# Kernel optimization log

Hardware: AMD Instinct MI355X
Metric: run time of the kernel (lower is better)

Reference implementation:

```python
import jax, jax.numpy as jnp
import numpy as np

BATCH, D_INNER, DT_RANK, N = 256, 5120, 160, 16

def _softplus_thresh(z, threshold=20.0):
    # softplus(z) with beta=1; linear above threshold (matches ttnn.softplus(parameter1=1, parameter2=20))
    return jnp.where(z > threshold, z, jax.nn.softplus(z))

def setup_inputs() -> dict:
    key = jax.random.key(0)
    ks = jax.random.split(key, 9)
    s = lambda d: 1.0 / np.sqrt(d)
    return {
        "x": jax.random.normal(ks[0], (1, 1, BATCH, D_INNER), jnp.float32),
        "h": jax.random.normal(ks[1], (BATCH, D_INNER, N), jnp.float32) * 0.1,
        "W_delta": jax.random.normal(ks[2], (D_INNER, DT_RANK), jnp.float32) * s(D_INNER),
        "W_dt": jax.random.normal(ks[3], (DT_RANK, D_INNER), jnp.float32) * s(DT_RANK),
        "b_dt": jax.random.normal(ks[4], (D_INNER,), jnp.float32) * 0.1,
        "A_log": jax.random.uniform(ks[5], (D_INNER, N), jnp.float32, 0.0, 1.5),
        "W_B": jax.random.normal(ks[6], (D_INNER, N), jnp.float32) * s(D_INNER),
        "W_C": jax.random.normal(ks[7], (D_INNER, N), jnp.float32) * s(D_INNER),
        "D": jax.random.normal(ks[8], (D_INNER,), jnp.float32),
    }

def reference(x, h, W_delta, W_dt, b_dt, A_log, W_B, W_C, D):
    # x: (1,1,B,d_inner) single decode step; h: (B,d_inner,n) SSM state
    xb = x.reshape(BATCH, D_INNER)                           # (B, d)
    # delta = softplus(x @ W_delta @ W_dt + b_dt)           -> (B, d)
    dt = _softplus_thresh((xb @ W_delta) @ W_dt + b_dt)
    A = -jnp.exp(A_log)                                      # (d, n)
    abar = jnp.exp(dt[:, :, None] * A[None, :, :])           # (B, d, n)
    Bp = xb @ W_B                                            # (B, n)
    # bbar * x: delta * B * x, broadcast over state dim
    bx = (dt * xb)[:, :, None] * Bp[:, None, :]              # (B, d, n)
    h_new = abar * h + bx                                    # (B, d, n) new hidden state
    C = xb @ W_C                                             # (B, n)
    y = jnp.einsum("bdn,bn->bd", h_new, C) + xb * D          # readout + skip (D)
    return y.reshape(1, 1, BATCH, D_INNER)
```

## Files before the change

kernel.cpp:

```cpp
#include <hip/hip_runtime.h>
#include <math.h>

#define BATCH 256
#define DIN   5120
#define RANK  160
#define NS    16
#define NCAT  192
#define NSPLIT 40

__global__ __launch_bounds__(256) void k1a_gemm(
    const float* __restrict__ x, const float* __restrict__ Wd,
    const float* __restrict__ WB, const float* __restrict__ WC,
    float* __restrict__ psum)
{
    __shared__ float xT[32][64];
    __shared__ float Wt[32][64];
    const int t  = threadIdx.x;
    const int m0 = blockIdx.x * 64;
    const int n0 = blockIdx.y * 64;
    const int z  = blockIdx.z;
    const int k0 = z * 128;
    const int tm = (t >> 4) * 4;
    const int tn = (t & 15) * 4;

    const int lm  = t >> 2;
    const int lk  = (t & 3) * 8;
    const int ln  = t & 63;
    const int lkb = (t >> 6) * 8;

    const float* wsrc; int wstr;
    {
        const int c = n0 + ln;
        if (c < RANK)            { wsrc = Wd + c;                wstr = RANK; }
        else if (c < RANK + NS)  { wsrc = WB + (c - RANK);       wstr = NS;   }
        else                     { wsrc = WC + (c - RANK - NS);  wstr = NS;   }
    }

    float acc[4][4] = {{0.f}};

    for (int ks = 0; ks < 4; ++ks) {
        const int kb = k0 + ks * 32;
        {
            const float* src = x + (size_t)(m0 + lm) * DIN + kb + lk;
            const float4 a0 = *(const float4*)src;
            const float4 a1 = *(const float4*)(src + 4);
            xT[lk+0][lm]=a0.x; xT[lk+1][lm]=a0.y; xT[lk+2][lm]=a0.z; xT[lk+3][lm]=a0.w;
            xT[lk+4][lm]=a1.x; xT[lk+5][lm]=a1.y; xT[lk+6][lm]=a1.z; xT[lk+7][lm]=a1.w;
        }
        {
            const float* wp = wsrc + (size_t)(kb + lkb) * wstr;
            #pragma unroll
            for (int i = 0; i < 8; ++i) { Wt[lkb + i][ln] = *wp; wp += wstr; }
        }
        __syncthreads();
        #pragma unroll
        for (int k = 0; k < 32; ++k) {
            const float4 a = *(const float4*)&xT[k][tm];
            const float4 b = *(const float4*)&Wt[k][tn];
            acc[0][0] += a.x*b.x; acc[0][1] += a.x*b.y; acc[0][2] += a.x*b.z; acc[0][3] += a.x*b.w;
            acc[1][0] += a.y*b.x; acc[1][1] += a.y*b.y; acc[1][2] += a.y*b.z; acc[1][3] += a.y*b.w;
            acc[2][0] += a.z*b.x; acc[2][1] += a.z*b.y; acc[2][2] += a.z*b.z; acc[2][3] += a.z*b.w;
            acc[3][0] += a.w*b.x; acc[3][1] += a.w*b.y; acc[3][2] += a.w*b.z; acc[3][3] += a.w*b.w;
        }
        __syncthreads();
    }

    float* dst = psum + (size_t)z * (BATCH * NCAT);
    #pragma unroll
    for (int i = 0; i < 4; ++i) {
        const int gm = m0 + tm + i;
        float4 o; o.x = acc[i][0]; o.y = acc[i][1]; o.z = acc[i][2]; o.w = acc[i][3];
        *(float4*)&dst[(size_t)gm * NCAT + n0 + tn] = o;
    }
}

__global__ __launch_bounds__(256) void k1r_reduce(
    const float* __restrict__ psum,
    float* __restrict__ P, float* __restrict__ Bp, float* __restrict__ Cc)
{
    const int o = blockIdx.x * 256 + threadIdx.x;
    float s = 0.f;
    #pragma unroll 8
    for (int z = 0; z < NSPLIT; ++z) s += psum[(size_t)z * (BATCH * NCAT) + o];
    const int gm = o / NCAT;
    const int gc = o - gm * NCAT;
    if (gc < RANK)           P [gm * RANK + gc]             = s;
    else if (gc < RANK + NS) Bp[gm * NS   + gc - RANK]      = s;
    else                     Cc[gm * NS   + gc - RANK - NS] = s;
}

__device__ __forceinline__ float softplus20(float z)
{
    if (z > 20.f) return z;
    return fmaxf(z, 0.f) + log1pf(__expf(-fabsf(z)));
}

__global__ __launch_bounds__(256) void k3_ssm(
    const float* __restrict__ P, const float* __restrict__ Wdt,
    const float* __restrict__ bdt, const float* __restrict__ x,
    const float* __restrict__ h, const float* __restrict__ A_log,
    const float* __restrict__ Bp, const float* __restrict__ Cc,
    const float* __restrict__ Dv, float* __restrict__ y)
{
    __shared__ float sP[16 * RANK];
    __shared__ float Bt[32][64];
    __shared__ float sdt[16][64];

    const int t    = threadIdx.x;
    const int lane = t & 63;
    const int wv   = t >> 6;
    const int c0   = blockIdx.x * 64;
    const int b0   = blockIdx.y * 16;

    {
        const float* Pb = P + (size_t)b0 * RANK;
        #pragma unroll
        for (int i = 0; i < 10; ++i) sP[i * 256 + t] = Pb[i * 256 + t];

        const int ln  = lane;
        const int lkb = wv * 8;
        float acc[4] = {0.f, 0.f, 0.f, 0.f};

        for (int ks = 0; ks < 5; ++ks) {
            const int kb = ks * 32;
            {
                const float* wp = Wdt + (size_t)(kb + lkb) * DIN + c0 + ln;
                #pragma unroll
                for (int i = 0; i < 8; ++i) Bt[lkb + i][ln] = wp[(size_t)i * DIN];
            }
            __syncthreads();
            #pragma unroll
            for (int k = 0; k < 32; ++k) {
                const float w = Bt[k][lane];
                acc[0] += sP[(wv * 4 + 0) * RANK + kb + k] * w;
                acc[1] += sP[(wv * 4 + 1) * RANK + kb + k] * w;
                acc[2] += sP[(wv * 4 + 2) * RANK + kb + k] * w;
                acc[3] += sP[(wv * 4 + 3) * RANK + kb + k] * w;
            }
            __syncthreads();
        }

        const float bz = bdt[c0 + lane];
        #pragma unroll
        for (int i = 0; i < 4; ++i)
            sdt[wv * 4 + i][lane] = softplus20(acc[i] + bz);
    }
    __syncthreads();

    const int v = lane & 3;
    const int j = lane >> 2;

    float4 A2q[4]; float dvq[4];
    #pragma unroll
    for (int q = 0; q < 4; ++q) {
        const int c = c0 + q * 16 + j;
        const float4 al = *(const float4*)(A_log + (size_t)c * NS + v * 4);
        A2q[q].x = -1.442695041f * __expf(al.x);
        A2q[q].y = -1.442695041f * __expf(al.y);
        A2q[q].z = -1.442695041f * __expf(al.z);
        A2q[q].w = -1.442695041f * __expf(al.w);
        dvq[q] = Dv[c];
    }

    #pragma unroll
    for (int g = 0; g < 2; ++g) {
        const int bl0 = wv * 4 + g * 2;
        const int gb0 = b0 + bl0;
        const int gb1 = gb0 + 1;

        const size_t hb0 = ((size_t)gb0 * DIN + c0) * NS;
        const size_t hb1 = ((size_t)gb1 * DIN + c0) * NS;
        const float4 h00 = *(const float4*)(h + hb0 +   0 + lane * 4);
        const float4 h01 = *(const float4*)(h + hb0 + 256 + lane * 4);
        const float4 h02 = *(const float4*)(h + hb0 + 512 + lane * 4);
        const float4 h03 = *(const float4*)(h + hb0 + 768 + lane * 4);
        const float4 h10 = *(const float4*)(h + hb1 +   0 + lane * 4);
        const float4 h11 = *(const float4*)(h + hb1 + 256 + lane * 4);
        const float4 h12 = *(const float4*)(h + hb1 + 512 + lane * 4);
        const float4 h13 = *(const float4*)(h + hb1 + 768 + lane * 4);
        const float  xr0 = x[(size_t)gb0 * DIN + c0 + lane];
        const float  xr1 = x[(size_t)gb1 * DIN + c0 + lane];
        const float4 B40 = *(const float4*)(Bp + gb0 * NS + v * 4);
        const float4 C40 = *(const float4*)(Cc + gb0 * NS + v * 4);
        const float4 B41 = *(const float4*)(Bp + gb1 * NS + v * 4);
        const float4 C41 = *(const float4*)(Cc + gb1 * NS + v * 4);

        float res0[4];
        #pragma unroll
        for (int q = 0; q < 4; ++q) {
            const float dtv = sdt[bl0][q * 16 + j];
            const float xv  = __shfl(xr0, q * 16 + j, 64);
            const float dtx = dtv * xv;
            const float4 hv = (q == 0) ? h00 : (q == 1) ? h01 : (q == 2) ? h02 : h03;
            float s;
            s  = (exp2f(dtv * A2q[q].x) * hv.x + dtx * B40.x) * C40.x;
            s += (exp2f(dtv * A2q[q].y) * hv.y + dtx * B40.y) * C40.y;
            s += (exp2f(dtv * A2q[q].z) * hv.z + dtx * B40.z) * C40.z;
            s += (exp2f(dtv * A2q[q].w) * hv.w + dtx * B40.w) * C40.w;
            if (v == 0) s += xv * dvq[q];
            res0[q] = s;
        }

        float res1[4];
        #pragma unroll
        for (int q = 0; q < 4; ++q) {
            const float dtv = sdt[bl0 + 1][q * 16 + j];
            const float xv  = __shfl(xr1, q * 16 + j, 64);
            const float dtx = dtv * xv;
            const float4 hv = (q == 0) ? h10 : (q == 1) ? h11 : (q == 2) ? h12 : h13;
            float s;
            s  = (exp2f(dtv * A2q[q].x) * hv.x + dtx * B41.x) * C41.x;
            s += (exp2f(dtv * A2q[q].y) * hv.y + dtx * B41.y) * C41.y;
            s += (exp2f(dtv * A2q[q].z) * hv.z + dtx * B41.z) * C41.z;
            s += (exp2f(dtv * A2q[q].w) * hv.w + dtx * B41.w) * C41.w;
            if (v == 0) s += xv * dvq[q];
            res1[q] = s;
        }

        #pragma unroll
        for (int q = 0; q < 4; ++q) {
            res0[q] += __shfl_xor(res0[q], 1, 64);
            res0[q] += __shfl_xor(res0[q], 2, 64);
            res1[q] += __shfl_xor(res1[q], 1, 64);
            res1[q] += __shfl_xor(res1[q], 2, 64);
        }
        const float out0 = (v == 0) ? res0[0] : (v == 1) ? res0[1]
                         : (v == 2) ? res0[2] : res0[3];
        const float out1 = (v == 0) ? res1[0] : (v == 1) ? res1[1]
                         : (v == 2) ? res1[2] : res1[3];
        y[(size_t)gb0 * DIN + c0 + v * 16 + j] = out0;
        y[(size_t)gb1 * DIN + c0 + v * 16 + j] = out1;
    }
}

extern "C" void kernel_launch(void* const* d_in, const int* in_sizes, int n_in,
                              void* d_out, int out_size, void* d_ws, size_t ws_size,
                              hipStream_t stream)
{
    const float* x     = (const float*)d_in[0];
    const float* h     = (const float*)d_in[1];
    const float* Wd    = (const float*)d_in[2];
    const float* Wdt   = (const float*)d_in[3];
    const float* bdt   = (const float*)d_in[4];
    const float* A_log = (const float*)d_in[5];
    const float* WB    = (const float*)d_in[6];
    const float* WC    = (const float*)d_in[7];
    const float* Dv    = (const float*)d_in[8];
    float* out = (float*)d_out;

    float* psum = (float*)d_ws;
    float* P    = psum + (size_t)NSPLIT * BATCH * NCAT;
    float* Bp   = P  + BATCH * RANK;
    float* Cc   = Bp + BATCH * NS;

    k1a_gemm  <<<dim3(4, 3, NSPLIT), 256, 0, stream>>>(x, Wd, WB, WC, psum);
    k1r_reduce<<<dim3(NCAT),         256, 0, stream>>>(psum, P, Bp, Cc);
    k3_ssm    <<<dim3(80, 16),       256, 0, stream>>>(P, Wdt, bdt, x, h, A_log,
                                                       Bp, Cc, Dv, out);
}
```

Measured before the change: 174.1 us.

## Split dt projection into its own tiled GEMM and slim the SSM kernel

Moves the P @ W_dt projection and softplus out of the SSM kernel into a separate register-tiled 64x64 GEMM that writes dt to workspace, reusing the psum buffer. Before, each of 16 batch blocks re-read W_dt per column tile. The SSM kernel now handles 2 batches per wave with no shared memory, giving a larger grid. The split-K factor of the first GEMM doubles and the reduce kernel uses smaller blocks to add parallelism. The cost is an extra launch and a round trip of dt through global memory.

```diff
diff --git a/kernel.cpp b/kernel.cpp
--- a/kernel.cpp
+++ b/kernel.cpp
@@ -6,7 +6,7 @@
 #define RANK  160
 #define NS    16
 #define NCAT  192
-#define NSPLIT 40
+#define NSPLIT 80
 
 __global__ __launch_bounds__(256) void k1a_gemm(
     const float* __restrict__ x, const float* __restrict__ Wd,
@@ -19,7 +19,7 @@
     const int m0 = blockIdx.x * 64;
     const int n0 = blockIdx.y * 64;
     const int z  = blockIdx.z;
-    const int k0 = z * 128;
+    const int k0 = z * 64;
     const int tm = (t >> 4) * 4;
     const int tn = (t & 15) * 4;
 
@@ -38,7 +38,7 @@
 
     float acc[4][4] = {{0.f}};
 
-    for (int ks = 0; ks < 4; ++ks) {
+    for (int ks = 0; ks < 2; ++ks) {
         const int kb = k0 + ks * 32;
         {
             const float* src = x + (size_t)(m0 + lm) * DIN + kb + lk;
@@ -74,11 +74,11 @@
     }
 }
 
-__global__ __launch_bounds__(256) void k1r_reduce(
+__global__ __launch_bounds__(128) void k1r_reduce(
     const float* __restrict__ psum,
     float* __restrict__ P, float* __restrict__ Bp, float* __restrict__ Cc)
 {
-    const int o = blockIdx.x * 256 + threadIdx.x;
+    const int o = blockIdx.x * 128 + threadIdx.x;
     float s = 0.f;
     #pragma unroll 8
     for (int z = 0; z < NSPLIT; ++z) s += psum[(size_t)z * (BATCH * NCAT) + o];
@@ -95,60 +95,98 @@
     return fmaxf(z, 0.f) + log1pf(__expf(-fabsf(z)));
 }
 
+__global__ __launch_bounds__(256) void k2_dt(
+    const float* __restrict__ P, const float* __restrict__ Wdt,
+    const float* __restrict__ bdt, float* __restrict__ dtw)
+{
+    __shared__ float aT[32][64];
+    __shared__ float Bt[32][64];
+
+    const int t  = threadIdx.x;
+    const int c0 = blockIdx.x * 64;
+    const int b0 = blockIdx.y * 64;
+
+    const int tm = (t >> 4) * 4;
+    const int tn = (t & 15) * 4;
+    const int lm  = t >> 2;
+    const int lk  = (t & 3) * 8;
+    const int ln  = t & 63;
+    const int lkb = (t >> 6) * 8;
+
+    float acc[4][4] = {{0.f}};
+
+    for (int ks = 0; ks < 5; ++ks) {
+        const int kb = ks * 32;
+        {
+            const float* src = P + (size_t)(b0 + lm) * RANK + kb + lk;
+            const float4 a0 = *(const float4*)src;
+            const float4 a1 = *(const float4*)(src + 4);
+            aT[lk+0][lm]=a0.x; aT[lk+1][lm]=a0.y; aT[lk+2][lm]=a0.z; aT[lk+3][lm]=a0.w;
+            aT[lk+4][lm]=a1.x; aT[lk+5][lm]=a1.y; aT[lk+6][lm]=a1.z; aT[lk+7][lm]=a1.w;
+        }
+        {
+            const float* wp = Wdt + (size_t)(kb + lkb) * DIN + c0 + ln;
+            #pragma unroll
+            for (int i = 0; i < 8; ++i) { Bt[lkb + i][ln] = wp[(size_t)i * DIN]; }
+        }
+        __syncthreads();
+        #pragma unroll
+        for (int k = 0; k < 32; ++k) {
+            const float4 a = *(const float4*)&aT[k][tm];
+            const float4 b = *(const float4*)&Bt[k][tn];
+            acc[0][0] += a.x*b.x; acc[0][1] += a.x*b.y; acc[0][2] += a.x*b.z; acc[0][3] += a.x*b.w;
+            acc[1][0] += a.y*b.x; acc[1][1] += a.y*b.y; acc[1][2] += a.y*b.z; acc[1][3] += a.y*b.w;
+            acc[2][0] += a.z*b.x; acc[2][1] += a.z*b.y; acc[2][2] += a.z*b.z; acc[2][3] += a.z*b.w;
+            acc[3][0] += a.w*b.x; acc[3][1] += a.w*b.y; acc[3][2] += a.w*b.z; acc[3][3] += a.w*b.w;
+        }
+        __syncthreads();
+    }
+
+    const float4 bz = *(const float4*)&bdt[c0 + tn];
+    #pragma unroll
+    for (int i = 0; i < 4; ++i) {
+        float4 o;
+        o.x = softplus20(acc[i][0] + bz.x);
+        o.y = softplus20(acc[i][1] + bz.y);
+        o.z = softplus20(acc[i][2] + bz.z);
+        o.w = softplus20(acc[i][3] + bz.w);
+        *(float4*)&dtw[(size_t)(b0 + tm + i) * DIN + c0 + tn] = o;
+    }
+}
+
 __global__ __launch_bounds__(256) void k3_ssm(
-    const float* __restrict__ P, const float* __restrict__ Wdt,
-    const float* __restrict__ bdt, const float* __restrict__ x,
+    const float* __restrict__ dtw, const float* __restrict__ x,
     const float* __restrict__ h, const float* __restrict__ A_log,
     const float* __restrict__ Bp, const float* __restrict__ Cc,
     const float* __restrict__ Dv, float* __restrict__ y)
 {
-    __shared__ float sP[16 * RANK];
-    __shared__ float Bt[32][64];
-    __shared__ float sdt[16][64];
-
     const int t    = threadIdx.x;
     const int lane = t & 63;
     const int wv   = t >> 6;
     const int c0   = blockIdx.x * 64;
-    const int b0   = blockIdx.y * 16;
-
-    {
-        const float* Pb = P + (size_t)b0 * RANK;
-        #pragma unroll
-        for (int i = 0; i < 10; ++i) sP[i * 256 + t] = Pb[i * 256 + t];
-
-        const int ln  = lane;
-        const int lkb = wv * 8;
-        float acc[4] = {0.f, 0.f, 0.f, 0.f};
-
-        for (int ks = 0; ks < 5; ++ks) {
-            const int kb = ks * 32;
-            {
-                const float* wp = Wdt + (size_t)(kb + lkb) * DIN + c0 + ln;
-                #pragma unroll
-                for (int i = 0; i < 8; ++i) Bt[lkb + i][ln] = wp[(size_t)i * DIN];
-            }
-            __syncthreads();
-            #pragma unroll
-            for (int k = 0; k < 32; ++k) {
-                const float w = Bt[k][lane];
-                acc[0] += sP[(wv * 4 + 0) * RANK + kb + k] * w;
-                acc[1] += sP[(wv * 4 + 1) * RANK + kb + k] * w;
-                acc[2] += sP[(wv * 4 + 2) * RANK + kb + k] * w;
-                acc[3] += sP[(wv * 4 + 3) * RANK + kb + k] * w;
-            }
-            __syncthreads();
-        }
-
-        const float bz = bdt[c0 + lane];
-        #pragma unroll
-        for (int i = 0; i < 4; ++i)
-            sdt[wv * 4 + i][lane] = softplus20(acc[i] + bz);
-    }
-    __syncthreads();
-
-    const int v = lane & 3;
-    const int j = lane >> 2;
+    const int gb0  = blockIdx.y * 8 + wv * 2;
+    const int gb1  = gb0 + 1;
+    const int v    = lane & 3;
+    const int j    = lane >> 2;
+
+    const size_t hb0 = ((size_t)gb0 * DIN + c0) * NS;
+    const size_t hb1 = ((size_t)gb1 * DIN + c0) * NS;
+    const float4 h00 = *(const float4*)(h + hb0 +   0 + lane * 4);
+    const float4 h01 = *(const float4*)(h + hb0 + 256 + lane * 4);
+    const float4 h02 = *(const float4*)(h + hb0 + 512 + lane * 4);
+    const float4 h03 = *(const float4*)(h + hb0 + 768 + lane * 4);
+    const float4 h10 = *(const float4*)(h + hb1 +   0 + lane * 4);
+    const float4 h11 = *(const float4*)(h + hb1 + 256 + lane * 4);
+    const float4 h12 = *(const float4*)(h + hb1 + 512 + lane * 4);
+    const float4 h13 = *(const float4*)(h + hb1 + 768 + lane * 4);
+    const float  xr0 = x  [(size_t)gb0 * DIN + c0 + lane];
+    const float  xr1 = x  [(size_t)gb1 * DIN + c0 + lane];
+    const float  dr0 = dtw[(size_t)gb0 * DIN + c0 + lane];
+    const float  dr1 = dtw[(size_t)gb1 * DIN + c0 + lane];
+    const float4 B40 = *(const float4*)(Bp + gb0 * NS + v * 4);
+    const float4 C40 = *(const float4*)(Cc + gb0 * NS + v * 4);
+    const float4 B41 = *(const float4*)(Bp + gb1 * NS + v * 4);
+    const float4 C41 = *(const float4*)(Cc + gb1 * NS + v * 4);
 
     float4 A2q[4]; float dvq[4];
     #pragma unroll
@@ -162,75 +200,51 @@
         dvq[q] = Dv[c];
     }
 
-    #pragma unroll
-    for (int g = 0; g < 2; ++g) {
-        const int bl0 = wv * 4 + g * 2;
-        const int gb0 = b0 + bl0;
-        const int gb1 = gb0 + 1;
-
-        const size_t hb0 = ((size_t)gb0 * DIN + c0) * NS;
-        const size_t hb1 = ((size_t)gb1 * DIN + c0) * NS;
-        const float4 h00 = *(const float4*)(h + hb0 +   0 + lane * 4);
-        const float4 h01 = *(const float4*)(h + hb0 + 256 + lane * 4);
-        const float4 h02 = *(const float4*)(h + hb0 + 512 + lane * 4);
-        const float4 h03 = *(const float4*)(h + hb0 + 768 + lane * 4);
-        const float4 h10 = *(const float4*)(h + hb1 +   0 + lane * 4);
-        const float4 h11 = *(const float4*)(h + hb1 + 256 + lane * 4);
-        const float4 h12 = *(const float4*)(h + hb1 + 512 + lane * 4);
-        const float4 h13 = *(const float4*)(h + hb1 + 768 + lane * 4);
-        const float  xr0 = x[(size_t)gb0 * DIN + c0 + lane];
-        const float  xr1 = x[(size_t)gb1 * DIN + c0 + lane];
-        const float4 B40 = *(const float4*)(Bp + gb0 * NS + v * 4);
-        const float4 C40 = *(const float4*)(Cc + gb0 * NS + v * 4);
-        const float4 B41 = *(const float4*)(Bp + gb1 * NS + v * 4);
-        const float4 C41 = *(const float4*)(Cc + gb1 * NS + v * 4);
-
-        float res0[4];
-        #pragma unroll
-        for (int q = 0; q < 4; ++q) {
-            const float dtv = sdt[bl0][q * 16 + j];
-            const float xv  = __shfl(xr0, q * 16 + j, 64);
-            const float dtx = dtv * xv;
-            const float4 hv = (q == 0) ? h00 : (q == 1) ? h01 : (q == 2) ? h02 : h03;
-            float s;
-            s  = (exp2f(dtv * A2q[q].x) * hv.x + dtx * B40.x) * C40.x;
-            s += (exp2f(dtv * A2q[q].y) * hv.y + dtx * B40.y) * C40.y;
-            s += (exp2f(dtv * A2q[q].z) * hv.z + dtx * B40.z) * C40.z;
-            s += (exp2f(dtv * A2q[q].w) * hv.w + dtx * B40.w) * C40.w;
-            if (v == 0) s += xv * dvq[q];
-            res0[q] = s;
-        }
-
-        float res1[4];
-        #pragma unroll
-        for (int q = 0; q < 4; ++q) {
-            const float dtv = sdt[bl0 + 1][q * 16 + j];
-            const float xv  = __shfl(xr1, q * 16 + j, 64);
-            const float dtx = dtv * xv;
-            const float4 hv = (q == 0) ? h10 : (q == 1) ? h11 : (q == 2) ? h12 : h13;
-            float s;
-            s  = (exp2f(dtv * A2q[q].x) * hv.x + dtx * B41.x) * C41.x;
-            s += (exp2f(dtv * A2q[q].y) * hv.y + dtx * B41.y) * C41.y;
-            s += (exp2f(dtv * A2q[q].z) * hv.z + dtx * B41.z) * C41.z;
-            s += (exp2f(dtv * A2q[q].w) * hv.w + dtx * B41.w) * C41.w;
-            if (v == 0) s += xv * dvq[q];
-            res1[q] = s;
-        }
-
-        #pragma unroll
-        for (int q = 0; q < 4; ++q) {
-            res0[q] += __shfl_xor(res0[q], 1, 64);
-            res0[q] += __shfl_xor(res0[q], 2, 64);
-            res1[q] += __shfl_xor(res1[q], 1, 64);
-            res1[q] += __shfl_xor(res1[q], 2, 64);
-        }
-        const float out0 = (v == 0) ? res0[0] : (v == 1) ? res0[1]
-                         : (v == 2) ? res0[2] : res0[3];
-        const float out1 = (v == 0) ? res1[0] : (v == 1) ? res1[1]
-                         : (v == 2) ? res1[2] : res1[3];
-        y[(size_t)gb0 * DIN + c0 + v * 16 + j] = out0;
-        y[(size_t)gb1 * DIN + c0 + v * 16 + j] = out1;
-    }
+    float res0[4];
+    #pragma unroll
+    for (int q = 0; q < 4; ++q) {
+        const float dtv = __shfl(dr0, q * 16 + j, 64);
+        const float xv  = __shfl(xr0, q * 16 + j, 64);
+        const float dtx = dtv * xv;
+        const float4 hv = (q == 0) ? h00 : (q == 1) ? h01 : (q == 2) ? h02 : h03;
+        float s;
+        s  = (exp2f(dtv * A2q[q].x) * hv.x + dtx * B40.x) * C40.x;
+        s += (exp2f(dtv * A2q[q].y) * hv.y + dtx * B40.y) * C40.y;
+        s += (exp2f(dtv * A2q[q].z) * hv.z + dtx * B40.z) * C40.z;
+        s += (exp2f(dtv * A2q[q].w) * hv.w + dtx * B40.w) * C40.w;
+        if (v == 0) s += xv * dvq[q];
+        res0[q] = s;
+    }
+
+    float res1[4];
+    #pragma unroll
+    for (int q = 0; q < 4; ++q) {
+        const float dtv = __shfl(dr1, q * 16 + j, 64);
+        const float xv  = __shfl(xr1, q * 16 + j, 64);
+        const float dtx = dtv * xv;
+        const float4 hv = (q == 0) ? h10 : (q == 1) ? h11 : (q == 2) ? h12 : h13;
+        float s;
+        s  = (exp2f(dtv * A2q[q].x) * hv.x + dtx * B41.x) * C41.x;
+        s += (exp2f(dtv * A2q[q].y) * hv.y + dtx * B41.y) * C41.y;
+        s += (exp2f(dtv * A2q[q].z) * hv.z + dtx * B41.z) * C41.z;
+        s += (exp2f(dtv * A2q[q].w) * hv.w + dtx * B41.w) * C41.w;
+        if (v == 0) s += xv * dvq[q];
+        res1[q] = s;
+    }
+
+    #pragma unroll
+    for (int q = 0; q < 4; ++q) {
+        res0[q] += __shfl_xor(res0[q], 1, 64);
+        res0[q] += __shfl_xor(res0[q], 2, 64);
+        res1[q] += __shfl_xor(res1[q], 1, 64);
+        res1[q] += __shfl_xor(res1[q], 2, 64);
+    }
+    const float out0 = (v == 0) ? res0[0] : (v == 1) ? res0[1]
+                     : (v == 2) ? res0[2] : res0[3];
+    const float out1 = (v == 0) ? res1[0] : (v == 1) ? res1[1]
+                     : (v == 2) ? res1[2] : res1[3];
+    y[(size_t)gb0 * DIN + c0 + v * 16 + j] = out0;
+    y[(size_t)gb1 * DIN + c0 + v * 16 + j] = out1;
 }
 
 extern "C" void kernel_launch(void* const* d_in, const int* in_sizes, int n_in,
@@ -249,12 +263,14 @@
     float* out = (float*)d_out;
 
     float* psum = (float*)d_ws;
+    float* dtw  = psum;
     float* P    = psum + (size_t)NSPLIT * BATCH * NCAT;
     float* Bp   = P  + BATCH * RANK;
     float* Cc   = Bp + BATCH * NS;
 
     k1a_gemm  <<<dim3(4, 3, NSPLIT), 256, 0, stream>>>(x, Wd, WB, WC, psum);
-    k1r_reduce<<<dim3(NCAT),         256, 0, stream>>>(psum, P, Bp, Cc);
-    k3_ssm    <<<dim3(80, 16),       256, 0, stream>>>(P, Wdt, bdt, x, h, A_log,
+    k1r_reduce<<<dim3(384),          128, 0, stream>>>(psum, P, Bp, Cc);
+    k2_dt     <<<dim3(80, 4),        256, 0, stream>>>(P, Wdt, bdt, dtw);
+    k3_ssm    <<<dim3(80, 32),       256, 0, stream>>>(dtw, x, h, A_log,
                                                        Bp, Cc, Dv, out);
 }
```

New measurement: 182.5 us. +4.9%, slower.
